# Performance work log

Hardware: AMD Instinct MI355X
Metric: run time of the kernel (lower is better)

The kernel has to match this reference:

```python
import jax, jax.numpy as jnp
import numpy as np

B, N, C_IN = 2, 2048, 256
H, C_H = 8, 32  # no_heads, c_hidden; H*C_H == 256


def setup_inputs() -> dict:
    key = jax.random.key(0)
    ks = jax.random.split(key, 10)
    s_in = 1.0 / np.sqrt(C_IN)
    s_hid = 1.0 / np.sqrt(H * C_H)
    return {
        "q_x": jax.random.normal(ks[0], (B, N, C_IN), dtype=jnp.float32),
        "kv_x": jax.random.normal(ks[1], (B, N, C_IN), dtype=jnp.float32),
        "bias": jax.random.normal(ks[2], (B, H, N, N), dtype=jnp.float32),
        # Linear weights stored as [in, out] (transpose of torch layout)
        "Wq": jax.random.normal(ks[3], (C_IN, H * C_H), dtype=jnp.float32) * s_in,
        "Wk": jax.random.normal(ks[4], (C_IN, H * C_H), dtype=jnp.float32) * s_in,
        "Wv": jax.random.normal(ks[5], (C_IN, H * C_H), dtype=jnp.float32) * s_in,
        "Wg": jax.random.normal(ks[6], (C_IN, H * C_H), dtype=jnp.float32) * s_in,
        "bg": jnp.zeros((H * C_H,), dtype=jnp.float32),
        "Wo": jax.random.normal(ks[7], (H * C_H, C_IN), dtype=jnp.float32) * s_hid,
        "bo": jnp.zeros((C_IN,), dtype=jnp.float32),
    }


def reference(q_x, kv_x, bias, Wq, Wk, Wv, Wg, bg, Wo, bo):
    inv_sqrt = 1.0 / jnp.sqrt(jnp.asarray(C_H, q_x.dtype))
    # projections -> [B, N, H, C_H]
    q = (q_x @ Wq).reshape(B, N, H, C_H) * inv_sqrt
    k = (kv_x @ Wk).reshape(B, N, H, C_H)
    v = (kv_x @ Wv).reshape(B, N, H, C_H)
    # attention scores [B, H, Nq, Nk] with added pairwise bias
    a = jnp.einsum("bqhc,bkhc->bhqk", q, k) + bias
    a = jax.nn.softmax(a, axis=-1)
    o = jnp.einsum("bhqk,bkhc->bqhc", a, v)  # [B, N, H, C_H]
    # sigmoid gating
    g = jax.nn.sigmoid(q_x @ Wg + bg).reshape(B, N, H, C_H)
    o = o * g
    # output projection
    return o.reshape(B, N, H * C_H) @ Wo + bo
```

## Files before the change

kernel.cpp:

```cpp
#include <hip/hip_runtime.h>
#include <hip/hip_bf16.h>

#define B_   2
#define N_   2048
#define CIN  256
#define NH   8
#define CH   32

typedef unsigned short u16;
typedef __attribute__((ext_vector_type(4))) float f32x4;
typedef __bf16 bf16x8 __attribute__((ext_vector_type(8)));
typedef u16 u16x4 __attribute__((ext_vector_type(4)));
typedef u16 u16x8 __attribute__((ext_vector_type(8)));

static __device__ __forceinline__ u16 b16(float f) {
    __bf16 h = (__bf16)f;
    union { __bf16 h; u16 u; } c; c.h = h; return c.u;
}
static __device__ __forceinline__ float bf2f(u16 u) {
    union { unsigned u; float f; } c; c.u = ((unsigned)u) << 16; return c.f;
}
static __device__ __forceinline__ float sigmoidf_(float x) {
    return 1.0f / (1.0f + __expf(-x));
}
static __device__ __forceinline__ void gload_lds16(const void* g, void* lds) {
    __builtin_amdgcn_global_load_lds(
        (const __attribute__((address_space(1))) unsigned int*)g,
        (__attribute__((address_space(3))) unsigned int*)lds, 16, 0, 0);
}

#define LDW 136

static __device__ __forceinline__ u16x8 cvt8(float4 a, float4 b) {
    u16x8 o;
    o[0] = b16(a.x); o[1] = b16(a.y); o[2] = b16(a.z); o[3] = b16(a.w);
    o[4] = b16(b.x); o[5] = b16(b.y); o[6] = b16(b.z); o[7] = b16(b.w);
    return o;
}
static __device__ __forceinline__ void stg_b16(const u16* __restrict__ src, u16 (*dst)[LDW], int tid) {
#pragma unroll
    for (int i = 0; i < 4; i++) {
        const int e = tid + 256 * i, row = e >> 4, c = e & 15;
        *(bf16x8*)&dst[row][c * 8] = *(const bf16x8*)(src + (size_t)row * CIN + c * 8);
    }
}
static __device__ __forceinline__ void ld1_b16(const u16* __restrict__ src, bf16x8 r[4], int tid) {
#pragma unroll
    for (int i = 0; i < 4; i++) {
        const int e = tid + 256 * i, row = e >> 4, c = e & 15;
        r[i] = *(const bf16x8*)(src + (size_t)row * CIN + 128 + c * 8);
    }
}
static __device__ __forceinline__ void wr1_b16(const bf16x8 r[4], u16 (*dst)[LDW], int tid) {
#pragma unroll
    for (int i = 0; i < 4; i++) {
        const int e = tid + 256 * i, row = e >> 4, c = e & 15;
        *(bf16x8*)&dst[row][c * 8] = r[i];
    }
}
static __device__ __forceinline__ void stg_f32(const float* __restrict__ src, u16 (*dst)[LDW], int tid) {
#pragma unroll
    for (int i = 0; i < 4; i++) {
        const int e = tid + 256 * i, row = e >> 4, c = e & 15;
        const float* s = src + (size_t)row * CIN + c * 8;
        *(u16x8*)&dst[row][c * 8] = cvt8(*(const float4*)s, *(const float4*)(s + 4));
    }
}
static __device__ __forceinline__ void trn_stage(const float* __restrict__ W, int n0,
                                                 u16 (*dst)[LDW], int tid, int kbase, float s) {
#pragma unroll
    for (int i = 0; i < 8; i++) {
        const int e = tid + 256 * i;
        const int kl = e >> 4;
        const int nb = e & 15;
#pragma unroll
        for (int j = 0; j < 4; j++) {
            float v = W[(size_t)(kbase + kl) * CIN + n0 + nb + j * 16];
            dst[nb + j * 16][kl] = b16(v * s);
        }
    }
}
static __device__ __forceinline__ void compute_phase(
    const u16 (*At)[LDW], const u16 (*Bt)[LDW], int w, int lr, int lq, f32x4 acc[4])
{
#pragma unroll
    for (int kk = 0; kk < 128; kk += 32) {
        bf16x8 af = *(const bf16x8*)&At[w * 16 + lr][kk + lq * 8];
#pragma unroll
        for (int nt = 0; nt < 4; nt++) {
            bf16x8 bf = *(const bf16x8*)&Bt[nt * 16 + lr][kk + lq * 8];
            acc[nt] = __builtin_amdgcn_mfma_f32_16x16x32_bf16(af, bf, acc[nt], 0, 0, 0);
        }
    }
}

__global__ __launch_bounds__(256, 4)
void proj_kernel(const float* __restrict__ qx, const float* __restrict__ kvx,
                 const float* __restrict__ Wq, const float* __restrict__ Wk,
                 const float* __restrict__ Wv, const float* __restrict__ Wg,
                 const float* __restrict__ bgv, const float* __restrict__ Wo,
                 u16* __restrict__ Qw, u16* __restrict__ Kw,
                 u16* __restrict__ Vt, u16* __restrict__ Gw,
                 u16* __restrict__ WoT, unsigned* __restrict__ rctr)
{
    const int flat = blockIdx.x;
    const int tid = threadIdx.x, w = tid >> 6, l = tid & 63, lr = l & 15, lq = l >> 4;
    __shared__ union {
        float T[64][65];
        struct { u16 At[64][LDW]; u16 Bt[64][LDW]; } g;
    } sh;

    if (flat >= 1024) {
        if (flat == 1024 && tid < 64) rctr[tid] = 0;
        const int t16 = flat - 1024;
        const int k0 = (t16 & 3) * 64, n0 = (t16 >> 2) * 64;
        const int a = tid >> 4, c4 = (tid & 15) * 4;
#pragma unroll
        for (int i = 0; i < 4; i++) {
            float4 v = *(const float4*)&Wo[(size_t)(k0 + a + i * 16) * CIN + n0 + c4];
            sh.T[a + i * 16][c4 + 0] = v.x; sh.T[a + i * 16][c4 + 1] = v.y;
            sh.T[a + i * 16][c4 + 2] = v.z; sh.T[a + i * 16][c4 + 3] = v.w;
        }
        __syncthreads();
#pragma unroll
        for (int i = 0; i < 4; i++) {
            const int nr = a + i * 16;
            u16x4 o;
            o[0] = b16(sh.T[c4 + 0][nr]); o[1] = b16(sh.T[c4 + 1][nr]);
            o[2] = b16(sh.T[c4 + 2][nr]); o[3] = b16(sh.T[c4 + 3][nr]);
            *(u16x4*)&WoT[(size_t)(n0 + nr) * CIN + k0 + c4] = o;
        }
        return;
    }

    const int z = flat >> 8, y = (flat >> 2) & 63, x = flat & 3;
    const float* Xf = ((z == 0 || z == 3) ? qx : kvx) + (size_t)(y * 64) * CIN;
    const float* Wz = (z == 0) ? Wq : (z == 1) ? Wk : (z == 2) ? Wv : Wg;
    const float scale = (z == 0) ? 0.17677669529663687f : 1.0f;
    const int n0w = x * 64;
    u16 (*Xt)[LDW] = (z == 2) ? sh.g.Bt : sh.g.At;
    u16 (*Wt)[LDW] = (z == 2) ? sh.g.At : sh.g.Bt;

    f32x4 acc[4] = {{0,0,0,0},{0,0,0,0},{0,0,0,0},{0,0,0,0}};

    stg_f32(Xf, Xt, tid);
    trn_stage(Wz, n0w, Wt, tid, 0, scale);
    __syncthreads();
    float4 rx[8];
#pragma unroll
    for (int i = 0; i < 4; i++) {
        const int e = tid + 256 * i, row = e >> 4, c = e & 15;
        const float* s = Xf + (size_t)row * CIN + 128 + c * 8;
        rx[2 * i] = *(const float4*)s; rx[2 * i + 1] = *(const float4*)(s + 4);
    }
    compute_phase(sh.g.At, sh.g.Bt, w, lr, lq, acc);
    __syncthreads();
#pragma unroll
    for (int i = 0; i < 4; i++) {
        const int e = tid + 256 * i, row = e >> 4, c = e & 15;
        *(u16x8*)&Xt[row][c * 8] = cvt8(rx[2 * i], rx[2 * i + 1]);
    }
    trn_stage(Wz, n0w, Wt, tid, 128, scale);
    __syncthreads();
    compute_phase(sh.g.At, sh.g.Bt, w, lr, lq, acc);

    if (z != 2) {
        const int m0 = y * 64 + w * 16, n0 = x * 64;
        if (z == 3) {
#pragma unroll
            for (int nt = 0; nt < 4; nt++) {
                const int col = n0 + nt * 16 + lr;
                const float bb = bgv[col];
#pragma unroll
                for (int r = 0; r < 4; r++)
                    Gw[(size_t)(m0 + lq * 4 + r) * CIN + col] = b16(sigmoidf_(acc[nt][r] + bb));
            }
        } else {
            u16* D = (z == 0) ? Qw : Kw;
#pragma unroll
            for (int nt = 0; nt < 4; nt++)
#pragma unroll
                for (int r = 0; r < 4; r++)
                    D[(size_t)(m0 + lq * 4 + r) * CIN + n0 + nt * 16 + lr] = b16(acc[nt][r]);
        }
    } else {
        const int c0 = x * 64 + w * 16;
        const int n0g = y * 64;
        const int bb_ = n0g >> 11, nl0 = n0g & (N_ - 1);
#pragma unroll
        for (int nt = 0; nt < 4; nt++)
#pragma unroll
            for (int r = 0; r < 4; r++)
                Vt[((size_t)bb_ * CIN + c0 + lq * 4 + r) * N_ + nl0 + nt * 16 + lr] = b16(acc[nt][r]);
    }
}

#define RMAX(x) { x = fmaxf(x, __shfl_xor(x, 1)); x = fmaxf(x, __shfl_xor(x, 2)); \
                  x = fmaxf(x, __shfl_xor(x, 4)); x = fmaxf(x, __shfl_xor(x, 8)); }
#define RSUM(x) { x += __shfl_xor(x, 1); x += __shfl_xor(x, 2); \
                  x += __shfl_xor(x, 4); x += __shfl_xor(x, 8); }

__global__ __launch_bounds__(256)
void attn_out_kernel(const u16* __restrict__ Qw, const u16* __restrict__ Kw,
                     const u16* __restrict__ Vt, const float* __restrict__ bias,
                     const u16* __restrict__ Gw, const u16* __restrict__ WoT,
                     const float* __restrict__ bo,
                     u16* __restrict__ Owg, float* __restrict__ out,
                     unsigned* __restrict__ rctr)
{
    const int bid = blockIdx.x;
    const int h = bid & 7, qt = (bid >> 3) & 31, b = bid >> 8;
    const int tid = threadIdx.x;
    const int w = tid >> 6, l = tid & 63, lr = l & 15, lq = l >> 4;
    const int qb = qt * 64;

    __shared__ union {
        struct { float Btl[4][3][16][32]; u16 Plds[4][8][4][16]; } a;
        struct { u16 At[64][LDW]; u16 Bt[64][LDW]; } g;
    } sh;
    __shared__ unsigned s_prev;

    const bf16x8 qf = *(const bf16x8*)(Qw + (size_t)(b * N_ + qb + w * 16 + lr) * CIN + h * CH + lq * 8);
    const u16* Kb = Kw + (size_t)(b * N_ + lr) * CIN + h * CH + lq * 8;
    const u16* Vb = Vt + (size_t)((b * NH + h) * CH + lr) * N_ + lq * 8;
    const float* biasW = bias + ((size_t)(b * NH + h) * N_ + qb + w * 16) * N_;
    const float* gl0 = biasW + (size_t)(l >> 3) * N_ + (l & 7) * 4;
    const float* gl1 = biasW + (size_t)(8 + (l >> 3)) * N_ + (l & 7) * 4;

#define STAGE(TT, BI) { \
    gload_lds16(gl0 + (size_t)(TT) * 32, &sh.a.Btl[w][BI][0][0]); \
    gload_lds16(gl1 + (size_t)(TT) * 32, &sh.a.Btl[w][BI][8][0]); }
#define KVLOAD(K) { kf0 = *(const bf16x8*)(Kb + (size_t)(K) * CIN); \
                    kf1 = *(const bf16x8*)(Kb + (size_t)((K) + 16) * CIN); \
                    vf0 = *(const bf16x8*)(Vb + (K)); \
                    vf1 = *(const bf16x8*)(Vb + 16 * N_ + (K)); }

    f32x4 acc0 = {0.f, 0.f, 0.f, 0.f}, acc1 = {0.f, 0.f, 0.f, 0.f};
    float m0v = 8.f, m1v = 8.f, m2v = 8.f, m3v = 8.f;
    float l0 = 0.f, l1 = 0.f, l2 = 0.f, l3 = 0.f;
    bf16x8 kf0, kf1, vf0, vf1;

    STAGE(0, 0)
    __builtin_amdgcn_sched_barrier(0);
    KVLOAD(0)
    __builtin_amdgcn_sched_barrier(0);
    STAGE(1, 1)
    __builtin_amdgcn_sched_barrier(0);

    int cur = 0, nxt = 2;
    for (int t = 0; t < 64; t++) {
        asm volatile("s_waitcnt vmcnt(2)" ::: "memory");
        const bf16x8 ck0 = kf0, ck1 = kf1, cv0 = vf0, cv1 = vf1;
        KVLOAD(((t + 1) & 63) * 32)
        __builtin_amdgcn_sched_barrier(0);
        STAGE((t + 2) & 63, nxt)
        __builtin_amdgcn_sched_barrier(0);

        const float* bt = &sh.a.Btl[w][cur][lq * 4][0];
        f32x4 c0, c1;
        c0[0] = bt[0 * 32 + lr];      c0[1] = bt[1 * 32 + lr];
        c0[2] = bt[2 * 32 + lr];      c0[3] = bt[3 * 32 + lr];
        c1[0] = bt[0 * 32 + 16 + lr]; c1[1] = bt[1 * 32 + 16 + lr];
        c1[2] = bt[2 * 32 + 16 + lr]; c1[3] = bt[3 * 32 + 16 + lr];

        f32x4 s0 = __builtin_amdgcn_mfma_f32_16x16x32_bf16(qf, ck0, c0, 0, 0, 0);
        f32x4 s1 = __builtin_amdgcn_mfma_f32_16x16x32_bf16(qf, ck1, c1, 0, 0, 0);

        float pm0 = fmaxf(s0[0], s1[0]);
        float pm1 = fmaxf(s0[1], s1[1]);
        float pm2 = fmaxf(s0[2], s1[2]);
        float pm3 = fmaxf(s0[3], s1[3]);
        bool ev = (pm0 > m0v) || (pm1 > m1v) || (pm2 > m2v) || (pm3 > m3v);
        if (__any(ev)) {
            RMAX(pm0) RMAX(pm1) RMAX(pm2) RMAX(pm3)
            float t0 = fmaxf(m0v, pm0), t1 = fmaxf(m1v, pm1);
            float t2 = fmaxf(m2v, pm2), t3 = fmaxf(m3v, pm3);
            float sc0 = __expf(m0v - t0), sc1 = __expf(m1v - t1);
            float sc2 = __expf(m2v - t2), sc3 = __expf(m3v - t3);
            m0v = t0; m1v = t1; m2v = t2; m3v = t3;
            l0 *= sc0; l1 *= sc1; l2 *= sc2; l3 *= sc3;
            acc0[0] *= sc0; acc0[1] *= sc1; acc0[2] *= sc2; acc0[3] *= sc3;
            acc1[0] *= sc0; acc1[1] *= sc1; acc1[2] *= sc2; acc1[3] *= sc3;
        }
        float p00 = __expf(s0[0] - m0v), p01 = __expf(s0[1] - m1v);
        float p02 = __expf(s0[2] - m2v), p03 = __expf(s0[3] - m3v);
        float p10 = __expf(s1[0] - m0v), p11 = __expf(s1[1] - m1v);
        float p12 = __expf(s1[2] - m2v), p13 = __expf(s1[3] - m3v);
        l0 += p00 + p10; l1 += p01 + p11; l2 += p02 + p12; l3 += p03 + p13;

        u16* pw = &sh.a.Plds[w][0][lq][lr];
        pw[0 * 64] = b16(p00); pw[1 * 64] = b16(p01);
        pw[2 * 64] = b16(p02); pw[3 * 64] = b16(p03);
        pw[4 * 64] = b16(p10); pw[5 * 64] = b16(p11);
        pw[6 * 64] = b16(p12); pw[7 * 64] = b16(p13);

        const bf16x8 pa = *(const bf16x8*)&sh.a.Plds[w][(lq >> 1) * 4 + (lr & 3)][lr >> 2][(lq & 1) * 8];
        acc0 = __builtin_amdgcn_mfma_f32_16x16x32_bf16(pa, cv0, acc0, 0, 0, 0);
        acc1 = __builtin_amdgcn_mfma_f32_16x16x32_bf16(pa, cv1, acc1, 0, 0, 0);

        cur = (cur == 2) ? 0 : cur + 1;
        nxt = (nxt == 2) ? 0 : nxt + 1;
    }
#undef STAGE
#undef KVLOAD

    RSUM(l0) RSUM(l1) RSUM(l2) RSUM(l3)
    const float rr[4] = {1.0f / l0, 1.0f / l1, 1.0f / l2, 1.0f / l3};
    const f32x4 a0 = acc0, a1 = acc1;

    const u16* Gb = Gw + (size_t)(b * N_ + qb + w * 16 + lq * 4) * CIN + h * CH + lr;
    u16* Ob = Owg + (size_t)(b * N_ + qb + w * 16 + lq * 4) * CIN + h * CH + lr;
#pragma unroll
    for (int r = 0; r < 4; r++) {
        const float g0 = bf2f(Gb[r * CIN]), g1 = bf2f(Gb[r * CIN + 16]);
        Ob[r * CIN]      = b16(a0[r] * rr[r] * g0);
        Ob[r * CIN + 16] = b16(a1[r] * rr[r] * g1);
    }

    asm volatile("s_waitcnt vmcnt(0)" ::: "memory");
    __syncthreads();
    if (tid == 0)
        s_prev = __hip_atomic_fetch_add(&rctr[b * 32 + qt], 1u,
                                        __ATOMIC_ACQ_REL, __HIP_MEMORY_SCOPE_AGENT);
    __syncthreads();
    if (s_prev != 7) return;

    const int y = b * 32 + qt;
    const u16* Arows = Owg + (size_t)(y * 64) * CIN;
    for (int x = 0; x < 4; x++) {
        const u16* Brows = WoT + (size_t)(x * 64) * CIN;
        f32x4 acc[4] = {{0,0,0,0},{0,0,0,0},{0,0,0,0},{0,0,0,0}};
        stg_b16(Arows, sh.g.At, tid);
        stg_b16(Brows, sh.g.Bt, tid);
        __syncthreads();
        bf16x8 ra[4], rb[4];
        ld1_b16(Arows, ra, tid);
        ld1_b16(Brows, rb, tid);
        compute_phase(sh.g.At, sh.g.Bt, w, lr, lq, acc);
        __syncthreads();
        wr1_b16(ra, sh.g.At, tid);
        wr1_b16(rb, sh.g.Bt, tid);
        __syncthreads();
        compute_phase(sh.g.At, sh.g.Bt, w, lr, lq, acc);

        const int m0 = y * 64 + w * 16, n0o = x * 64;
#pragma unroll
        for (int nt = 0; nt < 4; nt++) {
            const float bb = bo[n0o + nt * 16 + lr];
#pragma unroll
            for (int r = 0; r < 4; r++)
                out[(size_t)(m0 + lq * 4 + r) * CIN + n0o + nt * 16 + lr] = acc[nt][r] + bb;
        }
        __syncthreads();
    }
}

extern "C" void kernel_launch(void* const* d_in, const int* in_sizes, int n_in,
                              void* d_out, int out_size, void* d_ws, size_t ws_size,
                              hipStream_t stream)
{
    const float* qx   = (const float*)d_in[0];
    const float* kvx  = (const float*)d_in[1];
    const float* bias = (const float*)d_in[2];
    const float* Wq = (const float*)d_in[3];
    const float* Wk = (const float*)d_in[4];
    const float* Wv = (const float*)d_in[5];
    const float* Wg = (const float*)d_in[6];
    const float* bg = (const float*)d_in[7];
    const float* Wo = (const float*)d_in[8];
    const float* bo = (const float*)d_in[9];
    float* out = (float*)d_out;

    char* ws = (char*)d_ws;
    const size_t SZB = (size_t)B_ * N_ * CIN * 2;
    u16* Qw   = (u16*)(ws + 2 * SZB);
    u16* Kw   = (u16*)(ws + 3 * SZB);
    u16* Vt   = (u16*)(ws + 4 * SZB);
    u16* Gw   = (u16*)(ws + 5 * SZB);
    u16* Owg  = (u16*)(ws + 6 * SZB);
    const size_t WSZ = (size_t)CIN * CIN * 2;
    u16* WoT  = (u16*)(ws + 7 * SZB + 4 * WSZ);
    unsigned* rctr = (unsigned*)(ws + 7 * SZB + 5 * WSZ);

    proj_kernel<<<dim3(1040), 256, 0, stream>>>(qx, kvx, Wq, Wk, Wv, Wg, bg, Wo,
                                                Qw, Kw, Vt, Gw, WoT, rctr);
    attn_out_kernel<<<dim3(512), 256, 0, stream>>>(Qw, Kw, Vt, bias, Gw, WoT, bo,
                                                   Owg, out, rctr);
}
```

Before: 130.7 us.

## Split attention keys across waves, swizzle bias LDS, separate output projection kernel

The attention kernel now processes 32-query tiles, with pairs of waves splitting the 2048 keys in half. The two partial softmax states are merged through LDS, and the block count doubles to 1024 for more parallelism. The bias tile LDS layout gets an XOR swizzle to reduce bank conflicts. The fused last-block output projection with its atomic counter is replaced by a separate GEMM kernel launch, which trades an extra launch for removing the serialized tail work.

```diff
diff --git a/kernel.cpp b/kernel.cpp
--- a/kernel.cpp
+++ b/kernel.cpp
@@ -71,8 +71,7 @@
 #pragma unroll
     for (int i = 0; i < 8; i++) {
         const int e = tid + 256 * i;
-        const int kl = e >> 4;
-        const int nb = e & 15;
+        const int kl = e >> 4, nb = e & 15;
 #pragma unroll
         for (int j = 0; j < 4; j++) {
             float v = W[(size_t)(kbase + kl) * CIN + n0 + nb + j * 16];
@@ -101,7 +100,7 @@
                  const float* __restrict__ bgv, const float* __restrict__ Wo,
                  u16* __restrict__ Qw, u16* __restrict__ Kw,
                  u16* __restrict__ Vt, u16* __restrict__ Gw,
-                 u16* __restrict__ WoT, unsigned* __restrict__ rctr)
+                 u16* __restrict__ WoT)
 {
     const int flat = blockIdx.x;
     const int tid = threadIdx.x, w = tid >> 6, l = tid & 63, lr = l & 15, lq = l >> 4;
@@ -111,7 +110,6 @@
     } sh;
 
     if (flat >= 1024) {
-        if (flat == 1024 && tid < 64) rctr[tid] = 0;
         const int t16 = flat - 1024;
         const int k0 = (t16 & 3) * 64, n0 = (t16 >> 2) * 64;
         const int a = tid >> 4, c4 = (tid & 15) * 4;
@@ -201,35 +199,34 @@
                   x += __shfl_xor(x, 4); x += __shfl_xor(x, 8); }
 
 __global__ __launch_bounds__(256)
-void attn_out_kernel(const u16* __restrict__ Qw, const u16* __restrict__ Kw,
-                     const u16* __restrict__ Vt, const float* __restrict__ bias,
-                     const u16* __restrict__ Gw, const u16* __restrict__ WoT,
-                     const float* __restrict__ bo,
-                     u16* __restrict__ Owg, float* __restrict__ out,
-                     unsigned* __restrict__ rctr)
+void attn_kernel(const u16* __restrict__ Qw, const u16* __restrict__ Kw,
+                 const u16* __restrict__ Vt, const float* __restrict__ bias,
+                 const u16* __restrict__ Gw, u16* __restrict__ Owg)
 {
     const int bid = blockIdx.x;
-    const int h = bid & 7, qt = (bid >> 3) & 31, b = bid >> 8;
+    const int h = bid & 7, qt = (bid >> 3) & 63, b = bid >> 9;
     const int tid = threadIdx.x;
     const int w = tid >> 6, l = tid & 63, lr = l & 15, lq = l >> 4;
-    const int qb = qt * 64;
-
-    __shared__ union {
-        struct { float Btl[4][3][16][32]; u16 Plds[4][8][4][16]; } a;
-        struct { u16 At[64][LDW]; u16 Bt[64][LDW]; } g;
-    } sh;
-    __shared__ unsigned s_prev;
-
-    const bf16x8 qf = *(const bf16x8*)(Qw + (size_t)(b * N_ + qb + w * 16 + lr) * CIN + h * CH + lq * 8);
-    const u16* Kb = Kw + (size_t)(b * N_ + lr) * CIN + h * CH + lq * 8;
-    const u16* Vb = Vt + (size_t)((b * NH + h) * CH + lr) * N_ + lq * 8;
-    const float* biasW = bias + ((size_t)(b * NH + h) * N_ + qb + w * 16) * N_;
-    const float* gl0 = biasW + (size_t)(l >> 3) * N_ + (l & 7) * 4;
-    const float* gl1 = biasW + (size_t)(8 + (l >> 3)) * N_ + (l & 7) * 4;
+    const int rp = w & 1, kh = w >> 1;
+    const int qb = qt * 32;
+
+    __shared__ __align__(16) float Btl[4][3][16][32];
+    __shared__ u16 Plds[4][8][4][16];
+
+    const bf16x8 qf = *(const bf16x8*)(Qw + (size_t)(b * N_ + qb + rp * 16 + lr) * CIN + h * CH + lq * 8);
+    const u16* Kb = Kw + (size_t)(b * N_ + kh * 1024 + lr) * CIN + h * CH + lq * 8;
+    const u16* Vb = Vt + (size_t)((b * NH + h) * CH + lr) * N_ + kh * 1024 + lq * 8;
+    const float* biasW = bias + ((size_t)(b * NH + h) * N_ + qb + rp * 16) * N_ + kh * 1024;
+
+    const int brow0 = l >> 3;
+    const int cswz = ((l & 7) ^ (((l >> 3) & 4) ? 4 : 0)) * 4;
+    const float* gl0 = biasW + (size_t)brow0 * N_ + cswz;
+    const float* gl1 = biasW + (size_t)(8 + brow0) * N_ + cswz;
 
 #define STAGE(TT, BI) { \
-    gload_lds16(gl0 + (size_t)(TT) * 32, &sh.a.Btl[w][BI][0][0]); \
-    gload_lds16(gl1 + (size_t)(TT) * 32, &sh.a.Btl[w][BI][8][0]); }
+    gload_lds16(gl0 + (size_t)(TT) * 32, &Btl[w][BI][0][0]); \
+    gload_lds16(gl1 + (size_t)(TT) * 32, &Btl[w][BI][8][0]); }
+
 #define KVLOAD(K) { kf0 = *(const bf16x8*)(Kb + (size_t)(K) * CIN); \
                     kf1 = *(const bf16x8*)(Kb + (size_t)((K) + 16) * CIN); \
                     vf0 = *(const bf16x8*)(Vb + (K)); \
@@ -247,21 +244,22 @@
     STAGE(1, 1)
     __builtin_amdgcn_sched_barrier(0);
 
+    const int lrx = lr ^ ((lq & 1) << 4);
     int cur = 0, nxt = 2;
-    for (int t = 0; t < 64; t++) {
+    for (int t = 0; t < 32; t++) {
         asm volatile("s_waitcnt vmcnt(2)" ::: "memory");
         const bf16x8 ck0 = kf0, ck1 = kf1, cv0 = vf0, cv1 = vf1;
-        KVLOAD(((t + 1) & 63) * 32)
+        KVLOAD(((t + 1) & 31) * 32)
         __builtin_amdgcn_sched_barrier(0);
-        STAGE((t + 2) & 63, nxt)
+        STAGE((t + 2) & 31, nxt)
         __builtin_amdgcn_sched_barrier(0);
 
-        const float* bt = &sh.a.Btl[w][cur][lq * 4][0];
+        const float* bt = &Btl[w][cur][lq * 4][0];
         f32x4 c0, c1;
-        c0[0] = bt[0 * 32 + lr];      c0[1] = bt[1 * 32 + lr];
-        c0[2] = bt[2 * 32 + lr];      c0[3] = bt[3 * 32 + lr];
-        c1[0] = bt[0 * 32 + 16 + lr]; c1[1] = bt[1 * 32 + 16 + lr];
-        c1[2] = bt[2 * 32 + 16 + lr]; c1[3] = bt[3 * 32 + 16 + lr];
+        c0[0] = bt[0 * 32 + lrx];        c0[1] = bt[1 * 32 + lrx];
+        c0[2] = bt[2 * 32 + lrx];        c0[3] = bt[3 * 32 + lrx];
+        c1[0] = bt[0 * 32 + (lrx ^ 16)]; c1[1] = bt[1 * 32 + (lrx ^ 16)];
+        c1[2] = bt[2 * 32 + (lrx ^ 16)]; c1[3] = bt[3 * 32 + (lrx ^ 16)];
 
         f32x4 s0 = __builtin_amdgcn_mfma_f32_16x16x32_bf16(qf, ck0, c0, 0, 0, 0);
         f32x4 s1 = __builtin_amdgcn_mfma_f32_16x16x32_bf16(qf, ck1, c1, 0, 0, 0);
@@ -288,13 +286,13 @@
         float p12 = __expf(s1[2] - m2v), p13 = __expf(s1[3] - m3v);
         l0 += p00 + p10; l1 += p01 + p11; l2 += p02 + p12; l3 += p03 + p13;
 
-        u16* pw = &sh.a.Plds[w][0][lq][lr];
+        u16* pw = &Plds[w][0][lq][lr];
         pw[0 * 64] = b16(p00); pw[1 * 64] = b16(p01);
         pw[2 * 64] = b16(p02); pw[3 * 64] = b16(p03);
         pw[4 * 64] = b16(p10); pw[5 * 64] = b16(p11);
         pw[6 * 64] = b16(p12); pw[7 * 64] = b16(p13);
 
-        const bf16x8 pa = *(const bf16x8*)&sh.a.Plds[w][(lq >> 1) * 4 + (lr & 3)][lr >> 2][(lq & 1) * 8];
+        const bf16x8 pa = *(const bf16x8*)&Plds[w][(lq >> 1) * 4 + (lr & 3)][lr >> 2][(lq & 1) * 8];
         acc0 = __builtin_amdgcn_mfma_f32_16x16x32_bf16(pa, cv0, acc0, 0, 0, 0);
         acc1 = __builtin_amdgcn_mfma_f32_16x16x32_bf16(pa, cv1, acc1, 0, 0, 0);
 
@@ -305,53 +303,84 @@
 #undef KVLOAD
 
     RSUM(l0) RSUM(l1) RSUM(l2) RSUM(l3)
-    const float rr[4] = {1.0f / l0, 1.0f / l1, 1.0f / l2, 1.0f / l3};
-    const f32x4 a0 = acc0, a1 = acc1;
-
-    const u16* Gb = Gw + (size_t)(b * N_ + qb + w * 16 + lq * 4) * CIN + h * CH + lr;
-    u16* Ob = Owg + (size_t)(b * N_ + qb + w * 16 + lq * 4) * CIN + h * CH + lr;
+
+    asm volatile("s_waitcnt vmcnt(0)" ::: "memory");
+    float* P = (float*)&Btl[w][0][0][0];
+    if (kh == 1) {
+#pragma unroll
+        for (int r = 0; r < 4; r++) {
+            const int row = lq * 4 + r;
+            P[row * 32 + lr]      = acc0[r];
+            P[row * 32 + 16 + lr] = acc1[r];
+        }
+        if (lr == 0) {
+            P[512 + lq * 4 + 0] = m0v; P[512 + lq * 4 + 1] = m1v;
+            P[512 + lq * 4 + 2] = m2v; P[512 + lq * 4 + 3] = m3v;
+            P[528 + lq * 4 + 0] = l0;  P[528 + lq * 4 + 1] = l1;
+            P[528 + lq * 4 + 2] = l2;  P[528 + lq * 4 + 3] = l3;
+        }
+    }
+    __syncthreads();
+    if (kh == 1) return;
+
+    const float* PB = (const float*)&Btl[w + 2][0][0][0];
+    const float mA[4] = {m0v, m1v, m2v, m3v};
+    const float lA[4] = {l0, l1, l2, l3};
+
+    const u16* Gb = Gw + (size_t)(b * N_ + qb + rp * 16 + lq * 4) * CIN + h * CH + lr;
+    u16* Ob = Owg + (size_t)(b * N_ + qb + rp * 16 + lq * 4) * CIN + h * CH + lr;
 #pragma unroll
     for (int r = 0; r < 4; r++) {
+        const int row = lq * 4 + r;
+        const float mB = PB[512 + row];
+        const float lB = PB[528 + row];
+        const float ob0 = PB[row * 32 + lr];
+        const float ob1 = PB[row * 32 + 16 + lr];
+        const float mM = fmaxf(mA[r], mB);
+        const float sA = __expf(mA[r] - mM), sB = __expf(mB - mM);
+        const float rr = 1.0f / (lA[r] * sA + lB * sB);
+        const float a0 = (r == 0 ? acc0[0] : r == 1 ? acc0[1] : r == 2 ? acc0[2] : acc0[3]);
+        const float a1 = (r == 0 ? acc1[0] : r == 1 ? acc1[1] : r == 2 ? acc1[2] : acc1[3]);
         const float g0 = bf2f(Gb[r * CIN]), g1 = bf2f(Gb[r * CIN + 16]);
-        Ob[r * CIN]      = b16(a0[r] * rr[r] * g0);
-        Ob[r * CIN + 16] = b16(a1[r] * rr[r] * g1);
-    }
-
-    asm volatile("s_waitcnt vmcnt(0)" ::: "memory");
-    __syncthreads();
-    if (tid == 0)
-        s_prev = __hip_atomic_fetch_add(&rctr[b * 32 + qt], 1u,
-                                        __ATOMIC_ACQ_REL, __HIP_MEMORY_SCOPE_AGENT);
-    __syncthreads();
-    if (s_prev != 7) return;
-
-    const int y = b * 32 + qt;
-    const u16* Arows = Owg + (size_t)(y * 64) * CIN;
-    for (int x = 0; x < 4; x++) {
-        const u16* Brows = WoT + (size_t)(x * 64) * CIN;
-        f32x4 acc[4] = {{0,0,0,0},{0,0,0,0},{0,0,0,0},{0,0,0,0}};
-        stg_b16(Arows, sh.g.At, tid);
-        stg_b16(Brows, sh.g.Bt, tid);
-        __syncthreads();
-        bf16x8 ra[4], rb[4];
-        ld1_b16(Arows, ra, tid);
-        ld1_b16(Brows, rb, tid);
-        compute_phase(sh.g.At, sh.g.Bt, w, lr, lq, acc);
-        __syncthreads();
-        wr1_b16(ra, sh.g.At, tid);
-        wr1_b16(rb, sh.g.Bt, tid);
-        __syncthreads();
-        compute_phase(sh.g.At, sh.g.Bt, w, lr, lq, acc);
-
-        const int m0 = y * 64 + w * 16, n0o = x * 64;
-#pragma unroll
-        for (int nt = 0; nt < 4; nt++) {
-            const float bb = bo[n0o + nt * 16 + lr];
-#pragma unroll
-            for (int r = 0; r < 4; r++)
-                out[(size_t)(m0 + lq * 4 + r) * CIN + n0o + nt * 16 + lr] = acc[nt][r] + bb;
-        }
-        __syncthreads();
+        Ob[r * CIN]      = b16((a0 * sA + ob0 * sB) * rr * g0);
+        Ob[r * CIN + 16] = b16((a1 * sA + ob1 * sB) * rr * g1);
+    }
+}
+
+__global__ __launch_bounds__(256, 4)
+void out_mfma(const u16* __restrict__ Owg, const u16* __restrict__ WoT,
+              const float* __restrict__ bo, float* __restrict__ out)
+{
+    const int tid = threadIdx.x, w = tid >> 6, l = tid & 63, lr = l & 15, lq = l >> 4;
+    const int m0 = blockIdx.y * 64 + w * 16, n0 = blockIdx.x * 64;
+
+    __shared__ u16 At[64][LDW];
+    __shared__ u16 Bt[64][LDW];
+
+    const u16* Arows = Owg + (size_t)(blockIdx.y * 64) * CIN;
+    const u16* Brows = WoT + (size_t)(blockIdx.x * 64) * CIN;
+
+    f32x4 acc[4] = {{0,0,0,0},{0,0,0,0},{0,0,0,0},{0,0,0,0}};
+
+    stg_b16(Arows, At, tid);
+    stg_b16(Brows, Bt, tid);
+    __syncthreads();
+    bf16x8 ra[4], rb[4];
+    ld1_b16(Arows, ra, tid);
+    ld1_b16(Brows, rb, tid);
+    compute_phase(At, Bt, w, lr, lq, acc);
+    __syncthreads();
+    wr1_b16(ra, At, tid);
+    wr1_b16(rb, Bt, tid);
+    __syncthreads();
+    compute_phase(At, Bt, w, lr, lq, acc);
+
+#pragma unroll
+    for (int nt = 0; nt < 4; nt++) {
+        const float bb = bo[n0 + nt * 16 + lr];
+#pragma unroll
+        for (int r = 0; r < 4; r++)
+            out[(size_t)(m0 + lq * 4 + r) * CIN + n0 + nt * 16 + lr] = acc[nt][r] + bb;
     }
 }
 
@@ -380,10 +409,9 @@
     u16* Owg  = (u16*)(ws + 6 * SZB);
     const size_t WSZ = (size_t)CIN * CIN * 2;
     u16* WoT  = (u16*)(ws + 7 * SZB + 4 * WSZ);
-    unsigned* rctr = (unsigned*)(ws + 7 * SZB + 5 * WSZ);
 
     proj_kernel<<<dim3(1040), 256, 0, stream>>>(qx, kvx, Wq, Wk, Wv, Wg, bg, Wo,
-                                                Qw, Kw, Vt, Gw, WoT, rctr);
-    attn_out_kernel<<<dim3(512), 256, 0, stream>>>(Qw, Kw, Vt, bias, Gw, WoT, bo,
-                                                   Owg, out, rctr);
-}
+                                                Qw, Kw, Vt, Gw, WoT);
+    attn_kernel<<<dim3(1024), 256, 0, stream>>>(Qw, Kw, Vt, bias, Gw, Owg);
+    out_mfma<<<dim3(4, 64, 1), 256, 0, stream>>>(Owg, WoT, bo, out);
+}
```

Result: faster. 118.5 us (-9.4%).
